# Optimization experiments

Hardware: AMD Instinct MI355X
Metric: run time of the kernel (lower is better)

## Reference

```python
import jax, jax.numpy as jnp
import numpy as np


def setup_inputs() -> dict:
    key = jax.random.key(0)
    k1, k2, k3 = jax.random.split(key, 3)
    B, C, W, H, K = 8, 3, 512, 512, 13
    Wo, Ho = W - K + 1, H - K + 1
    return {
        "img": jax.random.normal(k1, (B, C, W, H), dtype=jnp.float32),
        "hori": jax.random.normal(k2, (B, K, Wo, Ho), dtype=jnp.float32),
        "vert": jax.random.normal(k3, (B, K, Wo, Ho), dtype=jnp.float32),
        "kernel_size": K,
    }


def reference(img, hori, vert, kernel_size):
    # out[b,c,i,j] = sum_{u,v} img[b,c,i+u,j+v] * vert[b,u,i,j] * hori[b,v,i,j]
    K = kernel_size
    B, C, W, H = img.shape
    Wo, Ho = W - K + 1, H - K + 1
    out = jnp.zeros((B, C, Wo, Ho), img.dtype)
    # Fixed small K x K loop over kernel taps; all pixel/batch dims vectorized.
    for v in range(K):
        h_v = hori[:, v][:, None]  # [B,1,Wo,Ho]
        acc = jnp.zeros((B, C, Wo, Ho), img.dtype)
        for u in range(K):
            acc = acc + img[:, :, u:u + Wo, v:v + Ho] * vert[:, u][:, None]
        out = out + acc * h_v
    return out
```

## Files before the change

### kernel.cpp

```cpp
#include <hip/hip_runtime.h>


#define KK 13
#define NB 8
#define NC 3
#define IW 512
#define IH 512
#define WO 500
#define HO 500
#define QROW 125
#define NT 384
#define NQ (KK * QROW)

typedef __attribute__((address_space(1))) const void g_void;
typedef __attribute__((address_space(3))) void l_void;

__global__ __launch_bounds__(NT) void sepconv_kernel(
    const float* __restrict__ img,
    const float* __restrict__ hori,
    const float* __restrict__ vert,
    float* __restrict__ out)
{
    __shared__ float4 s_vert[NQ];
    __shared__ float4 s_hori[NQ];

    const int tid = threadIdx.y * 128 + threadIdx.x;
    const int i = blockIdx.x;
    const int b = blockIdx.y;

    const size_t khw = (size_t)WO * HO;
    const size_t rs4 = khw / 4;
    const float4* vsrc = (const float4*)(vert + (size_t)b * KK * khw + (size_t)i * HO);
    const float4* hsrc = (const float4*)(hori + (size_t)b * KK * khw + (size_t)i * HO);

    #pragma unroll
    for (int f0 = 0; f0 < NQ; f0 += NT) {
        const int f = f0 + tid;
        if (f < NQ) {
            const unsigned u = (unsigned)f / QROW;
            const unsigned q = (unsigned)f - u * QROW;
            __builtin_amdgcn_global_load_lds(
                (g_void*)(vsrc + (size_t)u * rs4 + q),
                (l_void*)&s_vert[f], 16, 0, 0);
            __builtin_amdgcn_global_load_lds(
                (g_void*)(hsrc + (size_t)u * rs4 + q),
                (l_void*)&s_hori[f], 16, 0, 0);
        }
    }
    __syncthreads();

    const int tj = threadIdx.x;
    const int c  = threadIdx.y;
    if (tj >= QROW) return;
    const int j0 = tj * 4;

    const float* ibase = img + (((size_t)(b * NC + c) * IW) + i) * IH + j0;

    float tmp[4][KK];
    #pragma unroll
    for (int jq = 0; jq < 4; ++jq)
        #pragma unroll
        for (int v = 0; v < KK; ++v)
            tmp[jq][v] = 0.0f;

    float4 c0 = *(const float4*)(ibase + 0);
    float4 c1 = *(const float4*)(ibase + 4);
    float4 c2 = *(const float4*)(ibase + 8);
    float4 c3 = *(const float4*)(ibase + 12);

    #pragma unroll
    for (int u = 0; u < KK; ++u) {
        float4 n0, n1, n2, n3;
        if (u < KK - 1) {
            const float* rp = ibase + (size_t)(u + 1) * IH;
            n0 = *(const float4*)(rp + 0);
            n1 = *(const float4*)(rp + 4);
            n2 = *(const float4*)(rp + 8);
            n3 = *(const float4*)(rp + 12);
        }

        const float4 vt = s_vert[u * QROW + tj];

        float row[16];
        row[0]  = c0.x; row[1]  = c0.y; row[2]  = c0.z; row[3]  = c0.w;
        row[4]  = c1.x; row[5]  = c1.y; row[6]  = c1.z; row[7]  = c1.w;
        row[8]  = c2.x; row[9]  = c2.y; row[10] = c2.z; row[11] = c2.w;
        row[12] = c3.x; row[13] = c3.y; row[14] = c3.z; row[15] = c3.w;

        #pragma unroll
        for (int v = 0; v < KK; ++v) {
            tmp[0][v] += row[0 + v] * vt.x;
            tmp[1][v] += row[1 + v] * vt.y;
            tmp[2][v] += row[2 + v] * vt.z;
            tmp[3][v] += row[3 + v] * vt.w;
        }

        if (u < KK - 1) {
            c0 = n0; c1 = n1; c2 = n2; c3 = n3;
        }
    }

    float4 o = make_float4(0.f, 0.f, 0.f, 0.f);
    #pragma unroll
    for (int v = 0; v < KK; ++v) {
        const float4 hv = s_hori[v * QROW + tj];
        o.x += tmp[0][v] * hv.x;
        o.y += tmp[1][v] * hv.y;
        o.z += tmp[2][v] * hv.z;
        o.w += tmp[3][v] * hv.w;
    }

    float* op = out + (((size_t)(b * NC + c) * WO) + i) * HO + j0;
    *(float4*)op = o;
}

extern "C" void kernel_launch(void* const* d_in, const int* in_sizes, int n_in,
                              void* d_out, int out_size, void* d_ws, size_t ws_size,
                              hipStream_t stream) {
    const float* img  = (const float*)d_in[0];
    const float* hori = (const float*)d_in[1];
    const float* vert = (const float*)d_in[2];
    float* out = (float*)d_out;

    dim3 block(128, 3, 1);
    dim3 grid(WO, NB, 1);
    hipLaunchKernelGGL(sepconv_kernel, grid, block, 0, stream, img, hori, vert, out);
}
```

Measured before the change: 268.6 us.

## Load vert taps directly to registers and defer barrier until after accumulation

Drops the shared-memory staging of vert. Each thread now reads its vert float4 straight from global memory, with software prefetch two taps ahead. Only hori is still staged through LDS via async global_load_lds, and the __syncthreads is moved after the vertical accumulation, so the hori copy overlaps with compute instead of stalling before it. Launch bounds ask for 7 blocks per CU, which may raise register pressure. Vert values are no longer shared across the 3 channel rows, so each is loaded three times from global or cache.

Result: slower. 852.6 us (+217.5%).

```diff
diff --git a/kernel.cpp b/kernel.cpp
--- a/kernel.cpp
+++ b/kernel.cpp
@@ -15,13 +15,12 @@
 typedef __attribute__((address_space(1))) const void g_void;
 typedef __attribute__((address_space(3))) void l_void;
 
-__global__ __launch_bounds__(NT) void sepconv_kernel(
+__global__ __launch_bounds__(NT, 7) void sepconv_kernel(
     const float* __restrict__ img,
     const float* __restrict__ hori,
     const float* __restrict__ vert,
     float* __restrict__ out)
 {
-    __shared__ float4 s_vert[NQ];
     __shared__ float4 s_hori[NQ];
 
     const int tid = threadIdx.y * 128 + threadIdx.x;
@@ -37,24 +36,18 @@
     for (int f0 = 0; f0 < NQ; f0 += NT) {
         const int f = f0 + tid;
         if (f < NQ) {
-            const unsigned u = (unsigned)f / QROW;
-            const unsigned q = (unsigned)f - u * QROW;
+            const unsigned v = (unsigned)f / QROW;
+            const unsigned q = (unsigned)f - v * QROW;
             __builtin_amdgcn_global_load_lds(
-                (g_void*)(vsrc + (size_t)u * rs4 + q),
-                (l_void*)&s_vert[f], 16, 0, 0);
-            __builtin_amdgcn_global_load_lds(
-                (g_void*)(hsrc + (size_t)u * rs4 + q),
+                (g_void*)(hsrc + (size_t)v * rs4 + q),
                 (l_void*)&s_hori[f], 16, 0, 0);
         }
     }
-    __syncthreads();
 
     const int tj = threadIdx.x;
     const int c  = threadIdx.y;
-    if (tj >= QROW) return;
+    const bool active = (tj < QROW);
     const int j0 = tj * 4;
-
-    const float* ibase = img + (((size_t)(b * NC + c) * IW) + i) * IH + j0;
 
     float tmp[4][KK];
     #pragma unroll
@@ -63,55 +56,68 @@
         for (int v = 0; v < KK; ++v)
             tmp[jq][v] = 0.0f;
 
-    float4 c0 = *(const float4*)(ibase + 0);
-    float4 c1 = *(const float4*)(ibase + 4);
-    float4 c2 = *(const float4*)(ibase + 8);
-    float4 c3 = *(const float4*)(ibase + 12);
+    if (active) {
+        const float* ibase = img + (((size_t)(b * NC + c) * IW) + i) * IH + j0;
 
-    #pragma unroll
-    for (int u = 0; u < KK; ++u) {
-        float4 n0, n1, n2, n3;
-        if (u < KK - 1) {
-            const float* rp = ibase + (size_t)(u + 1) * IH;
-            n0 = *(const float4*)(rp + 0);
-            n1 = *(const float4*)(rp + 4);
-            n2 = *(const float4*)(rp + 8);
-            n3 = *(const float4*)(rp + 12);
-        }
-
-        const float4 vt = s_vert[u * QROW + tj];
-
-        float row[16];
-        row[0]  = c0.x; row[1]  = c0.y; row[2]  = c0.z; row[3]  = c0.w;
-        row[4]  = c1.x; row[5]  = c1.y; row[6]  = c1.z; row[7]  = c1.w;
-        row[8]  = c2.x; row[9]  = c2.y; row[10] = c2.z; row[11] = c2.w;
-        row[12] = c3.x; row[13] = c3.y; row[14] = c3.z; row[15] = c3.w;
+        float4 vt_c = vsrc[tj];
+        float4 vt_n = vsrc[rs4 + tj];
+        float4 c0 = *(const float4*)(ibase + 0);
+        float4 c1 = *(const float4*)(ibase + 4);
+        float4 c2 = *(const float4*)(ibase + 8);
+        float4 c3 = *(const float4*)(ibase + 12);
 
         #pragma unroll
-        for (int v = 0; v < KK; ++v) {
-            tmp[0][v] += row[0 + v] * vt.x;
-            tmp[1][v] += row[1 + v] * vt.y;
-            tmp[2][v] += row[2 + v] * vt.z;
-            tmp[3][v] += row[3 + v] * vt.w;
-        }
+        for (int u = 0; u < KK; ++u) {
+            float4 n0, n1, n2, n3, vt_nn;
+            if (u < KK - 1) {
+                const float* rp = ibase + (size_t)(u + 1) * IH;
+                n0 = *(const float4*)(rp + 0);
+                n1 = *(const float4*)(rp + 4);
+                n2 = *(const float4*)(rp + 8);
+                n3 = *(const float4*)(rp + 12);
+            }
+            if (u < KK - 2) {
+                vt_nn = vsrc[(size_t)(u + 2) * rs4 + tj];
+            }
 
-        if (u < KK - 1) {
-            c0 = n0; c1 = n1; c2 = n2; c3 = n3;
+            float row[16];
+            row[0]  = c0.x; row[1]  = c0.y; row[2]  = c0.z; row[3]  = c0.w;
+            row[4]  = c1.x; row[5]  = c1.y; row[6]  = c1.z; row[7]  = c1.w;
+            row[8]  = c2.x; row[9]  = c2.y; row[10] = c2.z; row[11] = c2.w;
+            row[12] = c3.x; row[13] = c3.y; row[14] = c3.z; row[15] = c3.w;
+
+            #pragma unroll
+            for (int v = 0; v < KK; ++v) {
+                tmp[0][v] += row[0 + v] * vt_c.x;
+                tmp[1][v] += row[1 + v] * vt_c.y;
+                tmp[2][v] += row[2 + v] * vt_c.z;
+                tmp[3][v] += row[3 + v] * vt_c.w;
+            }
+
+            if (u < KK - 1) {
+                c0 = n0; c1 = n1; c2 = n2; c3 = n3;
+            }
+            vt_c = vt_n;
+            vt_n = vt_nn;
         }
     }
 
-    float4 o = make_float4(0.f, 0.f, 0.f, 0.f);
-    #pragma unroll
-    for (int v = 0; v < KK; ++v) {
-        const float4 hv = s_hori[v * QROW + tj];
-        o.x += tmp[0][v] * hv.x;
-        o.y += tmp[1][v] * hv.y;
-        o.z += tmp[2][v] * hv.z;
-        o.w += tmp[3][v] * hv.w;
+    __syncthreads();
+
+    if (active) {
+        float4 o = make_float4(0.f, 0.f, 0.f, 0.f);
+        #pragma unroll
+        for (int v = 0; v < KK; ++v) {
+            const float4 hv = s_hori[v * QROW + tj];
+            o.x += tmp[0][v] * hv.x;
+            o.y += tmp[1][v] * hv.y;
+            o.z += tmp[2][v] * hv.z;
+            o.w += tmp[3][v] * hv.w;
+        }
+
+        float* op = out + (((size_t)(b * NC + c) * WO) + i) * HO + j0;
+        *(float4*)op = o;
     }
-
-    float* op = out + (((size_t)(b * NC + c) * WO) + i) * HO + j0;
-    *(float4*)op = o;
 }
 
 extern "C" void kernel_launch(void* const* d_in, const int* in_sizes, int n_in,
```

## Warp-specialize producer wave to double-buffer weight rows across four output rows

Applied to the files above, without the earlier changes.

Each block now handles four output rows and adds a dedicated producer wavefront. That wavefront streams the vert/hori weights for the next row into a double-buffered LDS area using global_load_lds, while the consumer waves compute the current row. The goal is to hide the weight-load latency that previously stalled every single-row block before its compute began. The handoff uses LDS atomics and spin-waits, and the grid shrinks to a quarter as many blocks, which adds synchronization overhead and reduces parallelism, including a risk of poor occupancy.

Measured after the change: 435.6 us. +62.2%, slower.

```diff
diff --git a/kernel.cpp b/kernel.cpp
--- a/kernel.cpp
+++ b/kernel.cpp
@@ -9,8 +9,11 @@
 #define WO 500
 #define HO 500
 #define QROW 125
-#define NT 384
-#define NQ (KK * QROW)
+#define RPB 4
+#define NCONS 384
+#define NT (NCONS + 64)
+#define NQ4 (2 * KK * QROW)
+#define NQPAD 3264
 
 typedef __attribute__((address_space(1))) const void g_void;
 typedef __attribute__((address_space(3))) void l_void;
@@ -21,97 +24,133 @@
     const float* __restrict__ vert,
     float* __restrict__ out)
 {
-    __shared__ float4 s_vert[NQ];
-    __shared__ float4 s_hori[NQ];
+    __shared__ float4 s_w[2][NQPAD];
+    __shared__ int ready_gen[2];
+    __shared__ int done_cnt[RPB];
 
-    const int tid = threadIdx.y * 128 + threadIdx.x;
-    const int i = blockIdx.x;
-    const int b = blockIdx.y;
+    const int tid = threadIdx.x;
+    const int b  = blockIdx.y;
+    const int i0 = blockIdx.x * RPB;
+
+    if (tid == 0) {
+        ready_gen[0] = -1; ready_gen[1] = -1;
+        #pragma unroll
+        for (int r = 0; r < RPB; ++r) done_cnt[r] = 0;
+    }
+    __syncthreads();
 
     const size_t khw = (size_t)WO * HO;
     const size_t rs4 = khw / 4;
-    const float4* vsrc = (const float4*)(vert + (size_t)b * KK * khw + (size_t)i * HO);
-    const float4* hsrc = (const float4*)(hori + (size_t)b * KK * khw + (size_t)i * HO);
 
-    #pragma unroll
-    for (int f0 = 0; f0 < NQ; f0 += NT) {
-        const int f = f0 + tid;
-        if (f < NQ) {
-            const unsigned u = (unsigned)f / QROW;
-            const unsigned q = (unsigned)f - u * QROW;
-            __builtin_amdgcn_global_load_lds(
-                (g_void*)(vsrc + (size_t)u * rs4 + q),
-                (l_void*)&s_vert[f], 16, 0, 0);
-            __builtin_amdgcn_global_load_lds(
-                (g_void*)(hsrc + (size_t)u * rs4 + q),
-                (l_void*)&s_hori[f], 16, 0, 0);
+    if (tid >= NCONS) {
+        const int lane = tid - NCONS;
+        const float4* vb0 = (const float4*)(vert + (size_t)b * KK * khw);
+        const float4* hb0 = (const float4*)(hori + (size_t)b * KK * khw);
+        for (int r = 0; r < RPB; ++r) {
+            if (r >= 2) {
+                while (__hip_atomic_load(&done_cnt[r - 2], __ATOMIC_ACQUIRE,
+                                         __HIP_MEMORY_SCOPE_WORKGROUP) < 6)
+                    __builtin_amdgcn_s_sleep(1);
+            }
+            const int bi = r & 1;
+            const float4* vb = vb0 + (size_t)(i0 + r) * QROW;
+            const float4* hb = hb0 + (size_t)(i0 + r) * QROW;
+            #pragma unroll
+            for (int s = 0; s < NQPAD / 64; ++s) {
+                const int f = s * 64 + lane;
+                int g = (f < KK * QROW) ? f : f - KK * QROW;
+                const float4* base = (f < KK * QROW) ? vb : hb;
+                if (f >= NQ4) { g = 0; base = vb; }
+                const unsigned u = (unsigned)g / QROW;
+                const unsigned q = (unsigned)g - u * QROW;
+                __builtin_amdgcn_global_load_lds(
+                    (g_void*)(base + (size_t)u * rs4 + q),
+                    (l_void*)&s_w[bi][f], 16, 0, 0);
+            }
+            asm volatile("s_waitcnt vmcnt(0)" ::: "memory");
+            __hip_atomic_store(&ready_gen[bi], r, __ATOMIC_RELEASE,
+                               __HIP_MEMORY_SCOPE_WORKGROUP);
         }
+        return;
     }
-    __syncthreads();
 
-    const int tj = threadIdx.x;
-    const int c  = threadIdx.y;
-    if (tj >= QROW) return;
+    const int tj = tid & 127;
+    const int c  = tid >> 7;
+    const bool active = (tj < QROW);
     const int j0 = tj * 4;
 
-    const float* ibase = img + (((size_t)(b * NC + c) * IW) + i) * IH + j0;
+    for (int r = 0; r < RPB; ++r) {
+        const int bi = r & 1;
+        while (__hip_atomic_load(&ready_gen[bi], __ATOMIC_ACQUIRE,
+                                 __HIP_MEMORY_SCOPE_WORKGROUP) < r)
+            __builtin_amdgcn_s_sleep(1);
 
-    float tmp[4][KK];
-    #pragma unroll
-    for (int jq = 0; jq < 4; ++jq)
+        float tmp[4][KK];
         #pragma unroll
-        for (int v = 0; v < KK; ++v)
-            tmp[jq][v] = 0.0f;
+        for (int jq = 0; jq < 4; ++jq)
+            #pragma unroll
+            for (int v = 0; v < KK; ++v)
+                tmp[jq][v] = 0.0f;
 
-    float4 c0 = *(const float4*)(ibase + 0);
-    float4 c1 = *(const float4*)(ibase + 4);
-    float4 c2 = *(const float4*)(ibase + 8);
-    float4 c3 = *(const float4*)(ibase + 12);
+        if (active) {
+            const int i = i0 + r;
+            const float* ibase = img + (((size_t)(b * NC + c) * IW) + i) * IH + j0;
 
-    #pragma unroll
-    for (int u = 0; u < KK; ++u) {
-        float4 n0, n1, n2, n3;
-        if (u < KK - 1) {
-            const float* rp = ibase + (size_t)(u + 1) * IH;
-            n0 = *(const float4*)(rp + 0);
-            n1 = *(const float4*)(rp + 4);
-            n2 = *(const float4*)(rp + 8);
-            n3 = *(const float4*)(rp + 12);
+            float4 c0 = *(const float4*)(ibase + 0);
+            float4 c1 = *(const float4*)(ibase + 4);
+            float4 c2 = *(const float4*)(ibase + 8);
+            float4 c3 = *(const float4*)(ibase + 12);
+
+            #pragma unroll
+            for (int u = 0; u < KK; ++u) {
+                float4 n0, n1, n2, n3;
+                if (u < KK - 1) {
+                    const float* rp = ibase + (size_t)(u + 1) * IH;
+                    n0 = *(const float4*)(rp + 0);
+                    n1 = *(const float4*)(rp + 4);
+                    n2 = *(const float4*)(rp + 8);
+                    n3 = *(const float4*)(rp + 12);
+                }
+
+                const float4 vt = s_w[bi][u * QROW + tj];
+
+                float row[16];
+                row[0]  = c0.x; row[1]  = c0.y; row[2]  = c0.z; row[3]  = c0.w;
+                row[4]  = c1.x; row[5]  = c1.y; row[6]  = c1.z; row[7]  = c1.w;
+                row[8]  = c2.x; row[9]  = c2.y; row[10] = c2.z; row[11] = c2.w;
+                row[12] = c3.x; row[13] = c3.y; row[14] = c3.z; row[15] = c3.w;
+
+                #pragma unroll
+                for (int v = 0; v < KK; ++v) {
+                    tmp[0][v] += row[0 + v] * vt.x;
+                    tmp[1][v] += row[1 + v] * vt.y;
+                    tmp[2][v] += row[2 + v] * vt.z;
+                    tmp[3][v] += row[3 + v] * vt.w;
+                }
+
+                if (u < KK - 1) {
+                    c0 = n0; c1 = n1; c2 = n2; c3 = n3;
+                }
+            }
+
+            float4 o = make_float4(0.f, 0.f, 0.f, 0.f);
+            #pragma unroll
+            for (int v = 0; v < KK; ++v) {
+                const float4 hv = s_w[bi][KK * QROW + v * QROW + tj];
+                o.x += tmp[0][v] * hv.x;
+                o.y += tmp[1][v] * hv.y;
+                o.z += tmp[2][v] * hv.z;
+                o.w += tmp[3][v] * hv.w;
+            }
+
+            float* op = out + (((size_t)(b * NC + c) * WO) + (size_t)(i0 + r)) * HO + j0;
+            *(float4*)op = o;
         }
 
-        const float4 vt = s_vert[u * QROW + tj];
-
-        float row[16];
-        row[0]  = c0.x; row[1]  = c0.y; row[2]  = c0.z; row[3]  = c0.w;
-        row[4]  = c1.x; row[5]  = c1.y; row[6]  = c1.z; row[7]  = c1.w;
-        row[8]  = c2.x; row[9]  = c2.y; row[10] = c2.z; row[11] = c2.w;
-        row[12] = c3.x; row[13] = c3.y; row[14] = c3.z; row[15] = c3.w;
-
-        #pragma unroll
-        for (int v = 0; v < KK; ++v) {
-            tmp[0][v] += row[0 + v] * vt.x;
-            tmp[1][v] += row[1 + v] * vt.y;
-            tmp[2][v] += row[2 + v] * vt.z;
-            tmp[3][v] += row[3 + v] * vt.w;
-        }
-
-        if (u < KK - 1) {
-            c0 = n0; c1 = n1; c2 = n2; c3 = n3;
-        }
+        if ((tid & 63) == 0)
+            __hip_atomic_fetch_add(&done_cnt[r], 1, __ATOMIC_RELEASE,
+                                   __HIP_MEMORY_SCOPE_WORKGROUP);
     }
-
-    float4 o = make_float4(0.f, 0.f, 0.f, 0.f);
-    #pragma unroll
-    for (int v = 0; v < KK; ++v) {
-        const float4 hv = s_hori[v * QROW + tj];
-        o.x += tmp[0][v] * hv.x;
-        o.y += tmp[1][v] * hv.y;
-        o.z += tmp[2][v] * hv.z;
-        o.w += tmp[3][v] * hv.w;
-    }
-
-    float* op = out + (((size_t)(b * NC + c) * WO) + i) * HO + j0;
-    *(float4*)op = o;
 }
 
 extern "C" void kernel_launch(void* const* d_in, const int* in_sizes, int n_in,
@@ -122,7 +161,7 @@
     const float* vert = (const float*)d_in[2];
     float* out = (float*)d_out;
 
-    dim3 block(128, 3, 1);
-    dim3 grid(WO, NB, 1);
+    dim3 block(NT, 1, 1);
+    dim3 grid(WO / RPB, NB, 1);
     hipLaunchKernelGGL(sepconv_kernel, grid, block, 0, stream, img, hori, vert, out);
 }
```

## Drop LDS staging, keep hori in registers and reorder sum order

Applied to the files above, without the earlier changes.

The kernel no longer stages the vert and hori rows into shared memory with a barrier. Each thread loads its 13 hori float4 values into registers and prefetches vert one row ahead. The summation order is swapped: the inner loop reduces over v with hori weights per image row, and vert is applied per row. This drops the 52-float tmp array in favour of 13 float4 registers. The block shrinks to 64x3 threads over a 2xWOxNB grid. The three channel threads now load the same hori and vert values redundantly, relying on caches, and the 2x64 split leaves some threads idle.

Result: slower. 309.2 us (+15.1%).

```diff
diff --git a/kernel.cpp b/kernel.cpp
--- a/kernel.cpp
+++ b/kernel.cpp
@@ -9,11 +9,8 @@
 #define WO 500
 #define HO 500
 #define QROW 125
-#define NT 384
-#define NQ (KK * QROW)
-
-typedef __attribute__((address_space(1))) const void g_void;
-typedef __attribute__((address_space(3))) void l_void;
+#define TJX 64
+#define NT (TJX * NC)
 
 __global__ __launch_bounds__(NT) void sepconv_kernel(
     const float* __restrict__ img,
@@ -21,56 +18,38 @@
     const float* __restrict__ vert,
     float* __restrict__ out)
 {
-    __shared__ float4 s_vert[NQ];
-    __shared__ float4 s_hori[NQ];
+    const int tj = blockIdx.x * TJX + threadIdx.x;
+    const int c  = threadIdx.y;
+    const int i  = blockIdx.y;
+    const int b  = blockIdx.z;
 
-    const int tid = threadIdx.y * 128 + threadIdx.x;
-    const int i = blockIdx.x;
-    const int b = blockIdx.y;
+    if (tj >= QROW) return;
+    const int j0 = tj * 4;
 
     const size_t khw = (size_t)WO * HO;
     const size_t rs4 = khw / 4;
-    const float4* vsrc = (const float4*)(vert + (size_t)b * KK * khw + (size_t)i * HO);
-    const float4* hsrc = (const float4*)(hori + (size_t)b * KK * khw + (size_t)i * HO);
 
+    const float4* hb = (const float4*)(hori + (size_t)b * KK * khw + (size_t)i * HO) + tj;
+    const float4* vb = (const float4*)(vert + (size_t)b * KK * khw + (size_t)i * HO) + tj;
+    const float*  ibase = img + (((size_t)(b * NC + c) * IW) + i) * IH + j0;
+
+    float4 h[KK];
     #pragma unroll
-    for (int f0 = 0; f0 < NQ; f0 += NT) {
-        const int f = f0 + tid;
-        if (f < NQ) {
-            const unsigned u = (unsigned)f / QROW;
-            const unsigned q = (unsigned)f - u * QROW;
-            __builtin_amdgcn_global_load_lds(
-                (g_void*)(vsrc + (size_t)u * rs4 + q),
-                (l_void*)&s_vert[f], 16, 0, 0);
-            __builtin_amdgcn_global_load_lds(
-                (g_void*)(hsrc + (size_t)u * rs4 + q),
-                (l_void*)&s_hori[f], 16, 0, 0);
-        }
-    }
-    __syncthreads();
+    for (int v = 0; v < KK; ++v)
+        h[v] = hb[(size_t)v * rs4];
 
-    const int tj = threadIdx.x;
-    const int c  = threadIdx.y;
-    if (tj >= QROW) return;
-    const int j0 = tj * 4;
-
-    const float* ibase = img + (((size_t)(b * NC + c) * IW) + i) * IH + j0;
-
-    float tmp[4][KK];
-    #pragma unroll
-    for (int jq = 0; jq < 4; ++jq)
-        #pragma unroll
-        for (int v = 0; v < KK; ++v)
-            tmp[jq][v] = 0.0f;
-
+    float4 vt_c = vb[0];
+    float4 vt_n = vb[rs4];
     float4 c0 = *(const float4*)(ibase + 0);
     float4 c1 = *(const float4*)(ibase + 4);
     float4 c2 = *(const float4*)(ibase + 8);
     float4 c3 = *(const float4*)(ibase + 12);
 
+    float4 o = make_float4(0.f, 0.f, 0.f, 0.f);
+
     #pragma unroll
     for (int u = 0; u < KK; ++u) {
-        float4 n0, n1, n2, n3;
+        float4 n0, n1, n2, n3, vt_nn;
         if (u < KK - 1) {
             const float* rp = ibase + (size_t)(u + 1) * IH;
             n0 = *(const float4*)(rp + 0);
@@ -78,8 +57,9 @@
             n2 = *(const float4*)(rp + 8);
             n3 = *(const float4*)(rp + 12);
         }
-
-        const float4 vt = s_vert[u * QROW + tj];
+        if (u < KK - 2) {
+            vt_nn = vb[(size_t)(u + 2) * rs4];
+        }
 
         float row[16];
         row[0]  = c0.x; row[1]  = c0.y; row[2]  = c0.z; row[3]  = c0.w;
@@ -87,27 +67,24 @@
         row[8]  = c2.x; row[9]  = c2.y; row[10] = c2.z; row[11] = c2.w;
         row[12] = c3.x; row[13] = c3.y; row[14] = c3.z; row[15] = c3.w;
 
+        float s0 = 0.f, s1 = 0.f, s2 = 0.f, s3 = 0.f;
         #pragma unroll
         for (int v = 0; v < KK; ++v) {
-            tmp[0][v] += row[0 + v] * vt.x;
-            tmp[1][v] += row[1 + v] * vt.y;
-            tmp[2][v] += row[2 + v] * vt.z;
-            tmp[3][v] += row[3 + v] * vt.w;
+            s0 += row[v + 0] * h[v].x;
+            s1 += row[v + 1] * h[v].y;
+            s2 += row[v + 2] * h[v].z;
+            s3 += row[v + 3] * h[v].w;
         }
+        o.x += vt_c.x * s0;
+        o.y += vt_c.y * s1;
+        o.z += vt_c.z * s2;
+        o.w += vt_c.w * s3;
 
         if (u < KK - 1) {
             c0 = n0; c1 = n1; c2 = n2; c3 = n3;
         }
-    }
-
-    float4 o = make_float4(0.f, 0.f, 0.f, 0.f);
-    #pragma unroll
-    for (int v = 0; v < KK; ++v) {
-        const float4 hv = s_hori[v * QROW + tj];
-        o.x += tmp[0][v] * hv.x;
-        o.y += tmp[1][v] * hv.y;
-        o.z += tmp[2][v] * hv.z;
-        o.w += tmp[3][v] * hv.w;
+        vt_c = vt_n;
+        vt_n = vt_nn;
     }
 
     float* op = out + (((size_t)(b * NC + c) * WO) + i) * HO + j0;
@@ -122,7 +99,7 @@
     const float* vert = (const float*)d_in[2];
     float* out = (float*)d_out;
 
-    dim3 block(128, 3, 1);
-    dim3 grid(WO, NB, 1);
+    dim3 block(TJX, NC, 1);
+    dim3 grid(2, WO, NB);
     hipLaunchKernelGGL(sepconv_kernel, grid, block, 0, stream, img, hori, vert, out);
 }
```
